# Performance work log

Measured on AMD Instinct MI355X. Metric: run time of the kernel, lower is better.

## Reference

```python
import jax, jax.numpy as jnp
import numpy as np

B, S, C = 16, 4096, 512


def setup_inputs() -> dict:
    key = jax.random.key(0)
    k1, k2, k3 = jax.random.split(key, 3)
    tag_logits_batch = jax.random.normal(k1, (B, S, C), dtype=jnp.float32)
    # probabilistic targets: normalize uniform draws so rows sum to 1
    t = jax.random.uniform(k2, (B, S, C), dtype=jnp.float32)
    target = t / jnp.sum(t, axis=-1, keepdims=True)
    mask = jax.random.randint(k3, (B, S), 0, 2, dtype=jnp.int32)
    return {"tag_logits_batch": tag_logits_batch, "target": target, "mask": mask}


def reference(tag_logits_batch, target, mask):
    # Soft-label cross-entropy per token: -sum_y target_y * log_softmax(logits)_y
    logp = jax.nn.log_softmax(tag_logits_batch, axis=-1)        # [B,S,C]
    tok_loss = -jnp.sum(target * logp, axis=-1)                  # [B,S]
    m = (mask == 1).astype(tok_loss.dtype)                       # [B,S]
    cnt = jnp.sum(m, axis=1)                                     # [B]
    # mean over active tokens per batch element (reduction='mean')
    per_batch = jnp.sum(tok_loss * m, axis=1) / jnp.maximum(cnt, 1.0)
    # torch code skips batch rows with no active tokens, then means over the rest
    has = (cnt > 0).astype(per_batch.dtype)                      # [B]
    return jnp.sum(per_batch * has) / jnp.maximum(jnp.sum(has), 1.0)
```

## Files before the change

### kernel.cpp

```cpp
#include <hip/hip_runtime.h>
#include <hip/hip_bf16.h>

#define BB 16
#define SS 4096
#define CC 512
#define NTOK (BB * SS)
#define LOSS_BLOCKS 2048
#define BLOCKS_PER_BATCH (LOSS_BLOCKS / BB)
#define WPB (BLOCKS_PER_BATCH * 4)


__global__ __launch_bounds__(256) void compact_kernel(
    const int* __restrict__ mask,
    int*       __restrict__ idxbuf,
    int*       __restrict__ cursors) {
    const int t     = blockIdx.x * 256 + threadIdx.x;
    const int batch = blockIdx.x / 16;
    const int lane  = threadIdx.x & 63;
    const int wave  = threadIdx.x >> 6;

    const bool active = (mask[t] == 1);
    unsigned long long ball = __ballot(active);
    const int prefix = __popcll(ball & ((1ull << lane) - 1ull));
    const int wcount = __popcll(ball);

    __shared__ int wbase[4];
    __shared__ int blockbase;
    if (lane == 0) wbase[wave] = wcount;
    __syncthreads();
    if (threadIdx.x == 0) {
        int total = wbase[0] + wbase[1] + wbase[2] + wbase[3];
        blockbase = atomicAdd(&cursors[batch], total);
        int s = 0;
        for (int i = 0; i < 4; ++i) { int c = wbase[i]; wbase[i] = s; s += c; }
    }
    __syncthreads();
    if (active)
        idxbuf[batch * SS + blockbase + wbase[wave] + prefix] = t;
}

__global__ __launch_bounds__(256, 8) void loss_kernel(
    const float* __restrict__ logits,
    const float* __restrict__ target,
    const int*   __restrict__ idxbuf,
    const int*   __restrict__ cursors,
    float*       __restrict__ partial) {
    const int wave  = threadIdx.x >> 6;
    const int lane  = threadIdx.x & 63;
    const int batch = blockIdx.x >> 7;
    const int wib   = (blockIdx.x & (BLOCKS_PER_BATCH - 1)) * 4 + wave;
    const int cnt   = cursors[batch];
    const int* list = idxbuf + batch * SS;

    float dotAcc = 0.0f;
    float logAcc = 0.0f;

    int k = wib;
    bool have = (k < cnt);
    float4 x0, x1, t0, t1;
    if (have) {
        const int tok = list[k];
        const float4* xp = (const float4*)(logits + (size_t)tok * CC);
        const float4* tp = (const float4*)(target + (size_t)tok * CC);
        x0 = xp[lane]; x1 = xp[lane + 64];
        t0 = tp[lane]; t1 = tp[lane + 64];
    }
    while (have) {
        const int kn = k + WPB;
        const bool haveN = (kn < cnt);
        float4 nx0, nx1, nt0, nt1;
        if (haveN) {
            const int tokN = list[kn];
            const float4* xp = (const float4*)(logits + (size_t)tokN * CC);
            const float4* tp = (const float4*)(target + (size_t)tokN * CC);
            nx0 = xp[lane]; nx1 = xp[lane + 64];
            nt0 = tp[lane]; nt1 = tp[lane + 64];
        }
        float se = __expf(x0.x) + __expf(x0.y) + __expf(x0.z) + __expf(x0.w)
                 + __expf(x1.x) + __expf(x1.y) + __expf(x1.z) + __expf(x1.w);
        dotAcc += t0.x * x0.x + t0.y * x0.y + t0.z * x0.z + t0.w * x0.w
                + t1.x * x1.x + t1.y * x1.y + t1.z * x1.z + t1.w * x1.w;
        #pragma unroll
        for (int off = 32; off >= 1; off >>= 1)
            se += __shfl_xor(se, off, 64);
        logAcc += __logf(se);
        x0 = nx0; x1 = nx1; t0 = nt0; t1 = nt1;
        k = kn; have = haveN;
    }

    #pragma unroll
    for (int off = 32; off >= 1; off >>= 1)
        dotAcc += __shfl_xor(dotAcc, off, 64);

    __shared__ float ls[4];
    if (lane == 0) ls[wave] = logAcc - dotAcc;
    __syncthreads();
    if (threadIdx.x == 0)
        partial[blockIdx.x] = ls[0] + ls[1] + ls[2] + ls[3];
}

__global__ __launch_bounds__(1024) void finalize_kernel(
    const float* __restrict__ partial,
    const int*   __restrict__ cursors,
    float*       __restrict__ out) {
    const int wave = threadIdx.x >> 6;
    const int lane = threadIdx.x & 63;

    float s = partial[wave * BLOCKS_PER_BATCH + lane]
            + partial[wave * BLOCKS_PER_BATCH + 64 + lane];
    #pragma unroll
    for (int off = 32; off >= 1; off >>= 1)
        s += __shfl_xor(s, off, 64);

    __shared__ float pb[BB], has[BB];
    if (lane == 0) {
        float c = (float)cursors[wave];
        pb[wave]  = (c > 0.0f) ? s / c : 0.0f;
        has[wave] = (c > 0.0f) ? 1.0f : 0.0f;
    }
    __syncthreads();
    if (threadIdx.x == 0) {
        float acc = 0.0f, nb = 0.0f;
        for (int b = 0; b < BB; ++b) { acc += pb[b]; nb += has[b]; }
        out[0] = acc / fmaxf(nb, 1.0f);
    }
}

extern "C" void kernel_launch(void* const* d_in, const int* in_sizes, int n_in,
                              void* d_out, int out_size, void* d_ws, size_t ws_size,
                              hipStream_t stream) {
    const float* logits = (const float*)d_in[0];
    const float* target = (const float*)d_in[1];
    const int*   mask   = (const int*)d_in[2];
    float* out     = (float*)d_out;
    int*   cursors = (int*)d_ws;
    int*   idxbuf  = (int*)((char*)d_ws + 128);
    float* partial = (float*)((char*)d_ws + 128 + NTOK * 4);

    hipMemsetAsync(cursors, 0, 64, stream);
    compact_kernel<<<NTOK / 256, 256, 0, stream>>>(mask, idxbuf, cursors);
    loss_kernel<<<LOSS_BLOCKS, 256, 0, stream>>>(logits, target, idxbuf, cursors, partial);
    finalize_kernel<<<1, 1024, 0, stream>>>(partial, cursors, out);
}
```

Before: 255.8 us.

## Stage token rows into LDS ring via async global_load_lds with persistent waves

```diff
diff --git a/kernel.cpp b/kernel.cpp
--- a/kernel.cpp
+++ b/kernel.cpp
@@ -1,14 +1,41 @@
 #include <hip/hip_runtime.h>
 #include <hip/hip_bf16.h>
+#include <stdint.h>
 
 #define BB 16
 #define SS 4096
 #define CC 512
 #define NTOK (BB * SS)
-#define LOSS_BLOCKS 2048
-#define BLOCKS_PER_BATCH (LOSS_BLOCKS / BB)
-#define WPB (BLOCKS_PER_BATCH * 4)
+#define LOSS_BLOCKS 768
+#define BPB (LOSS_BLOCKS / BB)
+#define WPBATCH (BPB * 4)
+#define GSTRIDE (WPBATCH * 4)
+#define MAXG 6
+#define DEPTH 3
+#define SLOT_F4 256
 
+
+#define WAITV(N) asm volatile("s_waitcnt vmcnt(" #N ")" ::: "memory")
+
+__device__ __forceinline__ void stage16(const void* g, void* l) {
+    auto* gp = reinterpret_cast<const uint32_t __attribute__((address_space(1)))*>(
+        reinterpret_cast<uintptr_t>(g));
+    auto* lp = reinterpret_cast<uint32_t __attribute__((address_space(3)))*>(
+        reinterpret_cast<uintptr_t>(l));
+    __builtin_amdgcn_global_load_lds(gp, lp, 16, 0, 0);
+}
+
+__device__ __forceinline__ void stage_token(const float* __restrict__ logits,
+                                            const float* __restrict__ target,
+                                            int tok, void* slot, int lane) {
+    const char* lrow = (const char*)(logits + (size_t)tok * CC) + lane * 16;
+    const char* trow = (const char*)(target + (size_t)tok * CC) + lane * 16;
+    char* s = (char*)slot;
+    stage16(lrow,        s);
+    stage16(lrow + 1024, s + 1024);
+    stage16(trow,        s + 2048);
+    stage16(trow + 1024, s + 3072);
+}
 
 __global__ __launch_bounds__(256) void compact_kernel(
     const int* __restrict__ mask,
@@ -39,43 +66,52 @@
         idxbuf[batch * SS + blockbase + wbase[wave] + prefix] = t;
 }
 
-__global__ __launch_bounds__(256, 8) void loss_kernel(
+__global__ __launch_bounds__(256) void loss_kernel(
     const float* __restrict__ logits,
     const float* __restrict__ target,
     const int*   __restrict__ idxbuf,
     const int*   __restrict__ cursors,
     float*       __restrict__ partial) {
+    __shared__ float4 ring[4][DEPTH][SLOT_F4];
+    __shared__ float  ls[4];
+
     const int wave  = threadIdx.x >> 6;
     const int lane  = threadIdx.x & 63;
-    const int batch = blockIdx.x >> 7;
-    const int wib   = (blockIdx.x & (BLOCKS_PER_BATCH - 1)) * 4 + wave;
+    const int batch = blockIdx.x / BPB;
+    const int wib   = (blockIdx.x % BPB) * 4 + wave;
     const int cnt   = cursors[batch];
     const int* list = idxbuf + batch * SS;
 
-    float dotAcc = 0.0f;
-    float logAcc = 0.0f;
+    int myidx = 0;
+    if (lane < 4 * MAXG)
+        myidx = list[wib * 4 + (lane >> 2) * GSTRIDE + (lane & 3)];
 
-    int k = wib;
-    bool have = (k < cnt);
-    float4 x0, x1, t0, t1;
-    if (have) {
-        const int tok = list[k];
-        const float4* xp = (const float4*)(logits + (size_t)tok * CC);
-        const float4* tp = (const float4*)(target + (size_t)tok * CC);
-        x0 = xp[lane]; x1 = xp[lane + 64];
-        t0 = tp[lane]; t1 = tp[lane + 64];
+    int nt = 0;
+    #pragma unroll
+    for (int g = 0; g < MAXG; ++g) {
+        int v = cnt - (wib * 4 + g * GSTRIDE);
+        nt += (v < 0) ? 0 : (v > 4 ? 4 : v);
     }
-    while (have) {
-        const int kn = k + WPB;
-        const bool haveN = (kn < cnt);
-        float4 nx0, nx1, nt0, nt1;
-        if (haveN) {
-            const int tokN = list[kn];
-            const float4* xp = (const float4*)(logits + (size_t)tokN * CC);
-            const float4* tp = (const float4*)(target + (size_t)tokN * CC);
-            nx0 = xp[lane]; nx1 = xp[lane + 64];
-            nt0 = tp[lane]; nt1 = tp[lane + 64];
+
+    if (nt > 0) stage_token(logits, target, __shfl(myidx, 0, 64), &ring[wave][0][0], lane);
+    if (nt > 1) stage_token(logits, target, __shfl(myidx, 1, 64), &ring[wave][1][0], lane);
+
+    float dotAcc = 0.0f, logAcc = 0.0f;
+    int s0 = 0, s2 = 2;
+    for (int i = 0; i < nt; ++i) {
+        if (i + 2 < nt) {
+            stage_token(logits, target, __shfl(myidx, i + 2, 64), &ring[wave][s2][0], lane);
+            WAITV(8);
+        } else if (i + 1 < nt) {
+            WAITV(4);
+        } else {
+            WAITV(0);
         }
+        const float4* sl = (const float4*)&ring[wave][s0][0];
+        float4 x0 = sl[lane];
+        float4 x1 = sl[lane + 64];
+        float4 t0 = sl[lane + 128];
+        float4 t1 = sl[lane + 192];
         float se = __expf(x0.x) + __expf(x0.y) + __expf(x0.z) + __expf(x0.w)
                  + __expf(x1.x) + __expf(x1.y) + __expf(x1.z) + __expf(x1.w);
         dotAcc += t0.x * x0.x + t0.y * x0.y + t0.z * x0.z + t0.w * x0.w
@@ -84,15 +120,14 @@
         for (int off = 32; off >= 1; off >>= 1)
             se += __shfl_xor(se, off, 64);
         logAcc += __logf(se);
-        x0 = nx0; x1 = nx1; t0 = nt0; t1 = nt1;
-        k = kn; have = haveN;
+        s0 = (s0 == 2) ? 0 : s0 + 1;
+        s2 = (s2 == 2) ? 0 : s2 + 1;
     }
 
     #pragma unroll
     for (int off = 32; off >= 1; off >>= 1)
         dotAcc += __shfl_xor(dotAcc, off, 64);
 
-    __shared__ float ls[4];
     if (lane == 0) ls[wave] = logAcc - dotAcc;
     __syncthreads();
     if (threadIdx.x == 0)
@@ -106,8 +141,7 @@
     const int wave = threadIdx.x >> 6;
     const int lane = threadIdx.x & 63;
 
-    float s = partial[wave * BLOCKS_PER_BATCH + lane]
-            + partial[wave * BLOCKS_PER_BATCH + 64 + lane];
+    float s = (lane < BPB) ? partial[wave * BPB + lane] : 0.0f;
     #pragma unroll
     for (int off = 32; off >= 1; off >>= 1)
         s += __shfl_xor(s, off, 64);
```

New measurement: 257.4 us. About the same (+0.6%).
